# Kernel tuning notes

Measured on AMD Instinct MI355X. Metric: run time of the kernel, lower is better.

Reference implementation:

```python
import jax, jax.numpy as jnp
import numpy as np

HIDDEN = 300
DEPTH = 6
ATOM_FDIM = 136
BOND_FDIM = 12
BOND_IN = ATOM_FDIM + BOND_FDIM  # 148
MAX_NB = 6
N_MOLS = 4096
ATOMS_PER_MOL = 32
N_ATOMS = N_MOLS * ATOMS_PER_MOL  # 131072
N_BONDS = 2 * N_ATOMS            # 262144 directed bonds


def setup_inputs() -> dict:
    key = jax.random.key(0)
    ks = jax.random.split(key, 11)
    fatoms = jax.random.normal(ks[0], (N_ATOMS, ATOM_FDIM), jnp.float32)
    fbonds = jax.random.normal(ks[1], (N_BONDS, BOND_IN), jnp.float32)
    agraph = jax.random.randint(ks[2], (N_ATOMS, MAX_NB), 0, N_BONDS, jnp.int32)
    bgraph = jax.random.randint(ks[3], (N_BONDS, MAX_NB), 0, N_BONDS, jnp.int32)
    # Linear weights stored pre-transposed so forward is x @ W
    W_i = jax.random.normal(ks[4], (BOND_IN, HIDDEN), jnp.float32) / np.sqrt(BOND_IN)
    W_h = jax.random.normal(ks[5], (HIDDEN, HIDDEN), jnp.float32) / np.sqrt(HIDDEN)
    W_o = jax.random.normal(ks[6], (ATOM_FDIM + HIDDEN, HIDDEN), jnp.float32) / np.sqrt(ATOM_FDIM + HIDDEN)
    b_o = jax.random.normal(ks[7], (HIDDEN,), jnp.float32) * 0.01
    W_a = jax.random.normal(ks[8], (HIDDEN, HIDDEN), jnp.float32) / np.sqrt(HIDDEN)
    W_b = jax.random.normal(ks[9], (HIDDEN, HIDDEN), jnp.float32) / np.sqrt(HIDDEN)
    b_b = jax.random.normal(ks[10], (HIDDEN,), jnp.float32) * 0.01
    return {"fatoms": fatoms, "fbonds": fbonds, "agraph": agraph, "bgraph": bgraph,
            "W_i": W_i, "W_h": W_h, "W_o": W_o, "b_o": b_o,
            "W_a": W_a, "W_b": W_b, "b_b": b_b}


def reference(fatoms, fbonds, agraph, bgraph, W_i, W_h, W_o, b_o, W_a, W_b, b_b):
    # D-MPNN bond message passing (dropout=0.0 -> identity)
    binput = fbonds @ W_i                         # [N_b, H]
    message = jax.nn.relu(binput)
    for _ in range(DEPTH - 1):
        nei = jnp.take(message, bgraph, axis=0).sum(axis=1)   # gather [N_b, MAX_NB, H] -> sum
        message = jax.nn.relu(binput + nei @ W_h)
    nei_a = jnp.take(message, agraph, axis=0).sum(axis=1)     # [N_a, H]
    atom_hiddens = jax.nn.relu(jnp.concatenate([fatoms, nei_a], axis=1) @ W_o + b_o)
    # Per-molecule self-attention pooling (fixed-size scope: ATOMS_PER_MOL atoms/mol)
    h = atom_hiddens.reshape(N_MOLS, ATOMS_PER_MOL, HIDDEN)   # [B, A, H]
    q = jnp.einsum('bah,hk->bak', h, W_a)
    att = jax.nn.softmax(jnp.einsum('bak,bck->bac', q, h), axis=-1)
    att_h = jax.nn.relu(jnp.einsum('bac,bch->bah', att, h) @ W_b + b_b)
    mol_vecs = (h + att_h).sum(axis=1) / ATOMS_PER_MOL        # [B, H]
    return mol_vecs
```

## Files before the change

### kernel.cpp

```cpp
#include <hip/hip_runtime.h>
#include <hip/hip_fp16.h>
#include <math.h>

#define HIDDEN 300
#define ATOM_FDIM 136
#define BOND_IN 148
#define MAX_NB 6
#define N_MOLS 4096
#define APM 32
#define N_ATOMS (N_MOLS*APM)
#define N_BONDS (2*N_ATOMS)

#define BK 16
#define BM 64
#define ASTR 68
#define BSTR 304

#define WT_C 304
#define WTK_H 320
#define WTK_O 448

typedef unsigned short u16;
typedef short bf16x8 __attribute__((ext_vector_type(8)));
typedef float f32x4  __attribute__((ext_vector_type(4)));

__device__ float g_scratch[3ull * N_BONDS * HIDDEN / 2 + 3ull * N_ATOMS * HIDDEN
                           + (size_t)N_MOLS * HIDDEN + WT_C * (WTK_H + WTK_O)];

__device__ __forceinline__ u16 bf16_rne(float x) {
    unsigned u = __float_as_uint(x);
    unsigned r = (u + 0x7fffu + ((u >> 16) & 1u)) >> 16;
    return (u16)r;
}
__device__ __forceinline__ float bf16_f(u16 h) {
    return __uint_as_float(((unsigned)h) << 16);
}
__device__ __forceinline__ void st_h4(__half* p, float a, float b, float c, float d) {
    *(__half2*)(p)     = __floats2half2_rn(a, b);
    *(__half2*)(p + 2) = __floats2half2_rn(c, d);
}

__global__ __launch_bounds__(256)
void wt_prep(const float* __restrict__ W, u16* __restrict__ hi_out,
             u16* __restrict__ lo_out, int kact, int wtk)
{
    const int i = blockIdx.x * 256 + threadIdx.x;
    if (i >= WT_C * wtk) return;
    const int c = i / wtk, k = i - c * wtk;
    float w = (c < HIDDEN && k < kact) ? W[(size_t)k * HIDDEN + c] : 0.f;
    const u16 hi = bf16_rne(w);
    const u16 lo = bf16_rne(w - bf16_f(hi));
    hi_out[i] = hi;
    lo_out[i] = lo;
}

__global__ __launch_bounds__(512)
void mp_mfma(const __half* __restrict__ msg,
             const int*   __restrict__ graph,
             const u16*   __restrict__ wt_hi,
             const u16*   __restrict__ wt_lo,
             const __half* __restrict__ binput,
             __half* __restrict__ out0)
{
    __shared__ u16 Ahi[64 * 40];
    __shared__ u16 Alo[64 * 40];
    __shared__ int gx[64 * MAX_NB];

    const int tid  = threadIdx.x;
    const int row0 = blockIdx.x * 64;

    if (tid < 64 * MAX_NB) gx[tid] = graph[(size_t)row0 * MAX_NB + tid];
    __syncthreads();

    const int w  = tid >> 6;
    const int l  = tid & 63;
    const int g  = l >> 4;
    const int mr = (w & 3) * 16 + (l & 15);
    const int tbase = (w >> 2) ? 10 : 0;
    const int ntile = (w >> 2) ? 9 : 10;

    const int sr = tid >> 3;
    const int sk = (tid & 7) * 4;
    const int* sg = &gx[sr * MAX_NB];

    f32x4 acc[10];
#pragma unroll
    for (int t = 0; t < 10; ++t) acc[t] = (f32x4){0.f, 0.f, 0.f, 0.f};

    for (int k0 = 0; k0 < HIDDEN; k0 += 32) {
        const int kk = k0 + sk;
        float s0 = 0.f, s1 = 0.f, s2 = 0.f, s3 = 0.f;
#pragma unroll
        for (int j = 0; j < MAX_NB; ++j) {
            const __half2* p = (const __half2*)(msg + (size_t)sg[j] * HIDDEN + kk);
            const float2 u = __half22float2(p[0]);
            const float2 v = __half22float2(p[1]);
            s0 += u.x; s1 += u.y; s2 += v.x; s3 += v.y;
        }
        const u16 h0 = bf16_rne(s0), h1 = bf16_rne(s1), h2 = bf16_rne(s2), h3 = bf16_rne(s3);
        const u16 e0 = bf16_rne(s0 - bf16_f(h0)), e1 = bf16_rne(s1 - bf16_f(h1));
        const u16 e2 = bf16_rne(s2 - bf16_f(h2)), e3 = bf16_rne(s3 - bf16_f(h3));
        uint2 ph, pl;
        ph.x = (unsigned)h0 | ((unsigned)h1 << 16);
        ph.y = (unsigned)h2 | ((unsigned)h3 << 16);
        pl.x = (unsigned)e0 | ((unsigned)e1 << 16);
        pl.y = (unsigned)e2 | ((unsigned)e3 << 16);
        *(uint2*)&Ahi[sr * 40 + sk] = ph;
        *(uint2*)&Alo[sr * 40 + sk] = pl;
        __syncthreads();

        const bf16x8 ahi = *(const bf16x8*)&Ahi[mr * 40 + 8 * g];
        const bf16x8 alo = *(const bf16x8*)&Alo[mr * 40 + 8 * g];
        const int kb = k0 + 8 * g;

#pragma unroll
        for (int t = 0; t < 10; ++t) {
            if (t < ntile) {
                const int cn = 16 * (tbase + t) + (l & 15);
                const bf16x8 bhi = *(const bf16x8*)&wt_hi[(size_t)cn * WTK_H + kb];
                const bf16x8 blo = *(const bf16x8*)&wt_lo[(size_t)cn * WTK_H + kb];
                acc[t] = __builtin_amdgcn_mfma_f32_16x16x32_bf16(ahi, bhi, acc[t], 0, 0, 0);
                acc[t] = __builtin_amdgcn_mfma_f32_16x16x32_bf16(ahi, blo, acc[t], 0, 0, 0);
                acc[t] = __builtin_amdgcn_mfma_f32_16x16x32_bf16(alo, bhi, acc[t], 0, 0, 0);
            }
        }
        __syncthreads();
    }

#pragma unroll
    for (int t = 0; t < 10; ++t) {
        if (t < ntile) {
            const int col = 16 * (tbase + t) + (l & 15);
            if (col < HIDDEN) {
#pragma unroll
                for (int j = 0; j < 4; ++j) {
                    const size_t off = (size_t)(row0 + (w & 3) * 16 + 4 * g + j) * HIDDEN + col;
                    out0[off] = __float2half(fmaxf(__half2float(binput[off]) + acc[t][j], 0.f));
                }
            }
        }
    }
}

__global__ __launch_bounds__(512)
void mo_mfma(const float* __restrict__ fatoms,
             const __half* __restrict__ msg,
             const int*   __restrict__ graph,
             const u16*   __restrict__ wto_hi,
             const u16*   __restrict__ wto_lo,
             const float* __restrict__ bias,
             float* __restrict__ out0)
{
    __shared__ u16 Ahi[64 * 40];
    __shared__ u16 Alo[64 * 40];
    __shared__ int gx[64 * MAX_NB];

    const int tid  = threadIdx.x;
    const int row0 = blockIdx.x * 64;

    if (tid < 64 * MAX_NB) gx[tid] = graph[(size_t)row0 * MAX_NB + tid];
    __syncthreads();

    const int w  = tid >> 6;
    const int l  = tid & 63;
    const int g  = l >> 4;
    const int mr = (w & 3) * 16 + (l & 15);
    const int tbase = (w >> 2) ? 10 : 0;
    const int ntile = (w >> 2) ? 9 : 10;

    const int sr = tid >> 3;
    const int sk = (tid & 7) * 4;
    const int* sg = &gx[sr * MAX_NB];
    const float* fa = fatoms + (size_t)(row0 + sr) * ATOM_FDIM;

    f32x4 acc[10];
#pragma unroll
    for (int t = 0; t < 10; ++t) acc[t] = (f32x4){0.f, 0.f, 0.f, 0.f};

    for (int k0 = 0; k0 < WTK_O; k0 += 32) {
        const int kk = k0 + sk;
        float s0, s1, s2, s3;
        if (kk + 4 <= ATOM_FDIM) {
            const float4 v = *(const float4*)&fa[kk];
            s0 = v.x; s1 = v.y; s2 = v.z; s3 = v.w;
        } else {
            const int kg = kk - ATOM_FDIM;
            s0 = 0.f; s1 = 0.f; s2 = 0.f; s3 = 0.f;
#pragma unroll
            for (int j = 0; j < MAX_NB; ++j) {
                const __half2* p = (const __half2*)(msg + (size_t)sg[j] * HIDDEN + kg);
                const float2 u = __half22float2(p[0]);
                const float2 v = __half22float2(p[1]);
                s0 += u.x; s1 += u.y; s2 += v.x; s3 += v.y;
            }
        }
        const u16 h0 = bf16_rne(s0), h1 = bf16_rne(s1), h2 = bf16_rne(s2), h3 = bf16_rne(s3);
        const u16 e0 = bf16_rne(s0 - bf16_f(h0)), e1 = bf16_rne(s1 - bf16_f(h1));
        const u16 e2 = bf16_rne(s2 - bf16_f(h2)), e3 = bf16_rne(s3 - bf16_f(h3));
        uint2 ph, pl;
        ph.x = (unsigned)h0 | ((unsigned)h1 << 16);
        ph.y = (unsigned)h2 | ((unsigned)h3 << 16);
        pl.x = (unsigned)e0 | ((unsigned)e1 << 16);
        pl.y = (unsigned)e2 | ((unsigned)e3 << 16);
        *(uint2*)&Ahi[sr * 40 + sk] = ph;
        *(uint2*)&Alo[sr * 40 + sk] = pl;
        __syncthreads();

        const bf16x8 ahi = *(const bf16x8*)&Ahi[mr * 40 + 8 * g];
        const bf16x8 alo = *(const bf16x8*)&Alo[mr * 40 + 8 * g];
        const int kb = k0 + 8 * g;

#pragma unroll
        for (int t = 0; t < 10; ++t) {
            if (t < ntile) {
                const int cn = 16 * (tbase + t) + (l & 15);
                const bf16x8 bhi = *(const bf16x8*)&wto_hi[(size_t)cn * WTK_O + kb];
                const bf16x8 blo = *(const bf16x8*)&wto_lo[(size_t)cn * WTK_O + kb];
                acc[t] = __builtin_amdgcn_mfma_f32_16x16x32_bf16(ahi, bhi, acc[t], 0, 0, 0);
                acc[t] = __builtin_amdgcn_mfma_f32_16x16x32_bf16(ahi, blo, acc[t], 0, 0, 0);
                acc[t] = __builtin_amdgcn_mfma_f32_16x16x32_bf16(alo, bhi, acc[t], 0, 0, 0);
            }
        }
        __syncthreads();
    }

#pragma unroll
    for (int t = 0; t < 10; ++t) {
        if (t < ntile) {
            const int col = 16 * (tbase + t) + (l & 15);
            if (col < HIDDEN) {
                const float bv = bias[col];
#pragma unroll
                for (int j = 0; j < 4; ++j) {
                    const size_t off = (size_t)(row0 + (w & 3) * 16 + 4 * g + j) * HIDDEN + col;
                    out0[off] = fmaxf(acc[t][j] + bv, 0.f);
                }
            }
        }
    }
}

template<int MODE>
__global__ __launch_bounds__(512)
void gemm_fused(const float* __restrict__ Adense, int lda,
                const float* __restrict__ W,
                const float* __restrict__ bias,
                const float* __restrict__ hsum,
                float* __restrict__ out0,
                float* __restrict__ out1,
                int K)
{
    __shared__ float As[BK * ASTR];
    __shared__ float Bs[BK * BSTR];

    const int tid  = threadIdx.x;
    const int wave = tid >> 6;
    const int lane = tid & 63;
    const int row0 = blockIdx.x * BM;
    const int c0   = 4 * lane;
    const bool has4 = (lane < HIDDEN - 256);
    const int  c4   = has4 ? (256 + lane) : 256;

    float acc[8][5];
#pragma unroll
    for (int r = 0; r < 8; ++r)
#pragma unroll
        for (int c = 0; c < 5; ++c) acc[r][c] = 0.f;

    const int nk = (K + BK - 1) / BK;
    for (int kt = 0; kt < nk; ++kt) {
        const int k0 = kt * BK;
        for (int i = tid; i < BK * 300; i += 512) {
            const int kk = i / 300;
            const int col = i - kk * 300;
            const int k = k0 + kk;
            Bs[kk * BSTR + col] = (k < K) ? W[(size_t)k * HIDDEN + col] : 0.f;
        }
        for (int i = tid; i < BK * BM; i += 512) {
            const int r  = i >> 4;
            const int kk = i & 15;
            const int k  = k0 + kk;
            As[kk * ASTR + r] = (k < K) ? Adense[(size_t)(row0 + r) * lda + k] : 0.f;
        }
        __syncthreads();
#pragma unroll
        for (int kk = 0; kk < BK; ++kk) {
            const float4 bq = *(const float4*)&Bs[kk * BSTR + c0];
            const float  b4 = Bs[kk * BSTR + c4];
            const float4 a0 = *(const float4*)&As[kk * ASTR + wave * 8];
            const float4 a1 = *(const float4*)&As[kk * ASTR + wave * 8 + 4];
            const float ar8[8] = {a0.x, a0.y, a0.z, a0.w, a1.x, a1.y, a1.z, a1.w};
#pragma unroll
            for (int r = 0; r < 8; ++r) {
                acc[r][0] = fmaf(ar8[r], bq.x, acc[r][0]);
                acc[r][1] = fmaf(ar8[r], bq.y, acc[r][1]);
                acc[r][2] = fmaf(ar8[r], bq.z, acc[r][2]);
                acc[r][3] = fmaf(ar8[r], bq.w, acc[r][3]);
                acc[r][4] = fmaf(ar8[r], b4,   acc[r][4]);
            }
        }
        __syncthreads();
    }

    if (MODE == 4) {
        const float4 bqv = *(const float4*)&bias[c0];
        const float  b4v = bias[c4];
        float s0 = 0, s1 = 0, s2 = 0, s3 = 0, s4 = 0;
#pragma unroll
        for (int r = 0; r < 8; ++r) {
            s0 += fmaxf(acc[r][0] + bqv.x, 0.f);
            s1 += fmaxf(acc[r][1] + bqv.y, 0.f);
            s2 += fmaxf(acc[r][2] + bqv.z, 0.f);
            s3 += fmaxf(acc[r][3] + bqv.w, 0.f);
            s4 += fmaxf(acc[r][4] + b4v,   0.f);
        }
        float* wsum = Bs;
        *(float4*)&wsum[wave * BSTR + c0] = make_float4(s0, s1, s2, s3);
        if (has4) wsum[wave * BSTR + c4] = s4;
        __syncthreads();
        const int m0 = blockIdx.x * 2;
        for (int t = tid; t < 2 * HIDDEN; t += 512) {
            const int m = t / HIDDEN, col = t - m * HIDDEN;
            const float v = wsum[(4 * m + 0) * BSTR + col] + wsum[(4 * m + 1) * BSTR + col]
                          + wsum[(4 * m + 2) * BSTR + col] + wsum[(4 * m + 3) * BSTR + col]
                          + hsum[(size_t)(m0 + m) * HIDDEN + col];
            out0[(size_t)(m0 + m) * HIDDEN + col] = v * (1.f / 32.f);
        }
        return;
    }

#pragma unroll
    for (int r = 0; r < 8; ++r) {
        const size_t off = (size_t)(row0 + wave * 8 + r) * HIDDEN;
        float4 v = make_float4(acc[r][0], acc[r][1], acc[r][2], acc[r][3]);
        float v4 = acc[r][4];
        if (MODE == 0) {
            __half* o0 = (__half*)out0;
            __half* o1 = (__half*)out1;
            st_h4(&o0[off + c0], v.x, v.y, v.z, v.w);
            if (has4) o0[off + c4] = __float2half(v4);
            st_h4(&o1[off + c0], fmaxf(v.x,0.f), fmaxf(v.y,0.f), fmaxf(v.z,0.f), fmaxf(v.w,0.f));
            if (has4) o1[off + c4] = __float2half(fmaxf(v4, 0.f));
        } else {
            *(float4*)&out0[off + c0] = v;
            if (has4) out0[off + c4] = v4;
        }
    }
}

#define HSTR 320

__device__ __forceinline__ int hsw(int a, int c4u) {
    return a * HSTR + ((c4u ^ (a & 7)) << 2);
}

__global__ __launch_bounds__(512)
void attn_mid(const float* __restrict__ atom_h,
              const float* __restrict__ q_all,
              float* __restrict__ P_all,
              float* __restrict__ hsum)
{
    __shared__ float hs[APM * HSTR];
    __shared__ float qs[APM * HIDDEN];
    __shared__ float att[APM][33];

    const int tid  = threadIdx.x;
    const int wave = tid >> 6;
    const int lane = tid & 63;
    const int mol  = blockIdx.x;
    const float* hb = atom_h + (size_t)mol * APM * HIDDEN;
    const float* qb = q_all  + (size_t)mol * APM * HIDDEN;

    for (int j = tid; j < APM * 75; j += 512) {
        const int a = j / 75, c4u = j - a * 75;
        *(float4*)&hs[hsw(a, c4u)] = *(const float4*)&hb[(size_t)a * HIDDEN + 4 * c4u];
    }
    for (int j = tid; j < APM * 75; j += 512)
        *(float4*)&qs[4 * j] = *(const float4*)&qb[4 * j];
    __syncthreads();

    {
        const int a = tid >> 5, b = tid & 31;
        float s0 = 0.f, s1 = 0.f;
        for (int t = 0; t < 75; ++t) {
            const float4 hv = *(const float4*)&hs[hsw(b, t)];
            const float4 q0 = *(const float4*)&qs[a * HIDDEN + 4 * t];
            const float4 q1 = *(const float4*)&qs[(a + 16) * HIDDEN + 4 * t];
            s0 = fmaf(q0.x, hv.x, fmaf(q0.y, hv.y, fmaf(q0.z, hv.z, fmaf(q0.w, hv.w, s0))));
            s1 = fmaf(q1.x, hv.x, fmaf(q1.y, hv.y, fmaf(q1.z, hv.z, fmaf(q1.w, hv.w, s1))));
        }
        att[a][b] = s0;
        att[a + 16][b] = s1;
    }
    __syncthreads();

    if (tid < APM) {
        float m = -3.4e38f;
#pragma unroll 4
        for (int b = 0; b < APM; ++b) m = fmaxf(m, att[tid][b]);
        float s = 0.f;
#pragma unroll 4
        for (int b = 0; b < APM; ++b) { const float e = __expf(att[tid][b] - m); att[tid][b] = e; s += e; }
        const float inv = 1.f / s;
#pragma unroll 4
        for (int b = 0; b < APM; ++b) att[tid][b] *= inv;
    }
    __syncthreads();

    {
        const int r0 = wave * 4;
        const int c0 = 4 * lane;
        const bool has4 = (lane < 44);
        const int c4u = 64 + (lane >> 2), c4r = lane & 3;
        float4 p[4];
        float  p4[4];
#pragma unroll
        for (int r = 0; r < 4; ++r) { p[r] = make_float4(0,0,0,0); p4[r] = 0.f; }
#pragma unroll 4
        for (int b = 0; b < APM; ++b) {
            const float4 hv = *(const float4*)&hs[hsw(b, lane)];
            const float  h4 = hs[hsw(b, c4u) + c4r];
#pragma unroll
            for (int r = 0; r < 4; ++r) {
                const float av = att[r0 + r][b];
                p[r].x = fmaf(av, hv.x, p[r].x);
                p[r].y = fmaf(av, hv.y, p[r].y);
                p[r].z = fmaf(av, hv.z, p[r].z);
                p[r].w = fmaf(av, hv.w, p[r].w);
                p4[r]  = fmaf(av, h4,   p4[r]);
            }
        }
#pragma unroll
        for (int r = 0; r < 4; ++r) {
            const size_t off = ((size_t)mol * APM + r0 + r) * HIDDEN;
            *(float4*)&P_all[off + c0] = p[r];
            if (has4) P_all[off + 256 + lane] = p4[r];
        }
    }

    if (tid < HIDDEN) {
        const int c4u = tid >> 2, cr = tid & 3;
        float s = 0.f;
#pragma unroll 4
        for (int a = 0; a < APM; ++a) s += hs[hsw(a, c4u) + cr];
        hsum[(size_t)mol * HIDDEN + tid] = s;
    }
}

extern "C" void kernel_launch(void* const* d_in, const int* in_sizes, int n_in,
                              void* d_out, int out_size, void* d_ws, size_t ws_size,
                              hipStream_t stream)
{
    const float* fatoms = (const float*)d_in[0];
    const float* fbonds = (const float*)d_in[1];
    const int*   agraph = (const int*)d_in[2];
    const int*   bgraph = (const int*)d_in[3];
    const float* W_i    = (const float*)d_in[4];
    const float* W_h    = (const float*)d_in[5];
    const float* W_o    = (const float*)d_in[6];
    const float* b_o    = (const float*)d_in[7];
    const float* W_a    = (const float*)d_in[8];
    const float* W_b    = (const float*)d_in[9];
    const float* b_b    = (const float*)d_in[10];
    float* out = (float*)d_out;

    const size_t WB = (size_t)N_BONDS * HIDDEN;
    const size_t WA = (size_t)N_ATOMS * HIDDEN;
    const size_t need = (3 * WB / 2 + 3 * WA + (size_t)N_MOLS * HIDDEN
                         + WT_C * (WTK_H + WTK_O)) * sizeof(float);
    float* base;
    if (ws_size >= need) {
        base = (float*)d_ws;
    } else {
        void* p = nullptr;
        (void)hipGetSymbolAddress(&p, HIP_SYMBOL(g_scratch));
        base = (float*)p;
    }
    __half* binput_h = (__half*)base;
    __half* msgA     = (__half*)(base + WB / 2);
    __half* msgB     = (__half*)(base + WB);
    float*  atom_h   = base + 3 * WB / 2;
    float*  q_all    = atom_h + WA;
    float*  P_all    = q_all + WA;
    float*  hsum     = P_all + WA;
    u16*    wt_hi    = (u16*)(hsum + (size_t)N_MOLS * HIDDEN);
    u16*    wt_lo    = wt_hi + WT_C * WTK_H;
    u16*    wto_hi   = wt_lo + WT_C * WTK_H;
    u16*    wto_lo   = wto_hi + WT_C * WTK_O;

    const dim3 blk(512);

    wt_prep<<<(WT_C * WTK_H + 255) / 256, dim3(256), 0, stream>>>(
        W_h, wt_hi, wt_lo, HIDDEN, WTK_H);
    wt_prep<<<(WT_C * WTK_O + 255) / 256, dim3(256), 0, stream>>>(
        W_o, wto_hi, wto_lo, ATOM_FDIM + HIDDEN, WTK_O);

    gemm_fused<0><<<N_BONDS / BM, blk, 0, stream>>>(
        fbonds, BOND_IN, W_i, nullptr, nullptr,
        (float*)binput_h, (float*)msgA, BOND_IN);

    const __half* cur = msgA;
    __half* nxt = msgB;
    for (int it = 0; it < 5; ++it) {
        mp_mfma<<<N_BONDS / 64, blk, 0, stream>>>(
            cur, bgraph, wt_hi, wt_lo, binput_h, nxt);
        __half* t = nxt; nxt = (__half*)cur; cur = t;
    }

    mo_mfma<<<N_ATOMS / 64, blk, 0, stream>>>(
        fatoms, cur, agraph, wto_hi, wto_lo, b_o, atom_h);

    gemm_fused<3><<<N_ATOMS / BM, blk, 0, stream>>>(
        atom_h, HIDDEN, W_a, nullptr, nullptr,
        q_all, nullptr, HIDDEN);

    attn_mid<<<N_MOLS, dim3(512), 0, stream>>>(atom_h, q_all, P_all, hsum);

    gemm_fused<4><<<N_ATOMS / BM, blk, 0, stream>>>(
        P_all, HIDDEN, W_b, b_b, hsum,
        out, nullptr, HIDDEN);
}
```

Baseline: 6.711 ms.

## Replace FP32 SIMT GEMMs with split-bf16 MFMA kernels for W_i, W_a, W_b

```diff
diff --git a/kernel.cpp b/kernel.cpp
--- a/kernel.cpp
+++ b/kernel.cpp
@@ -11,21 +11,17 @@
 #define N_ATOMS (N_MOLS*APM)
 #define N_BONDS (2*N_ATOMS)
 
-#define BK 16
-#define BM 64
-#define ASTR 68
-#define BSTR 304
-
 #define WT_C 304
 #define WTK_H 320
 #define WTK_O 448
+#define WTK_I 160
 
 typedef unsigned short u16;
 typedef short bf16x8 __attribute__((ext_vector_type(8)));
 typedef float f32x4  __attribute__((ext_vector_type(4)));
 
 __device__ float g_scratch[3ull * N_BONDS * HIDDEN / 2 + 3ull * N_ATOMS * HIDDEN
-                           + (size_t)N_MOLS * HIDDEN + WT_C * (WTK_H + WTK_O)];
+                           + (size_t)N_MOLS * HIDDEN + 476672];
 
 __device__ __forceinline__ u16 bf16_rne(float x) {
     unsigned u = __float_as_uint(x);
@@ -34,10 +30,6 @@
 }
 __device__ __forceinline__ float bf16_f(u16 h) {
     return __uint_as_float(((unsigned)h) << 16);
-}
-__device__ __forceinline__ void st_h4(__half* p, float a, float b, float c, float d) {
-    *(__half2*)(p)     = __floats2half2_rn(a, b);
-    *(__half2*)(p + 2) = __floats2half2_rn(c, d);
 }
 
 __global__ __launch_bounds__(256)
@@ -54,6 +46,18 @@
     lo_out[i] = lo;
 }
 
+__device__ __forceinline__ void split4(float s0, float s1, float s2, float s3,
+                                       uint2& ph, uint2& pl)
+{
+    const u16 h0 = bf16_rne(s0), h1 = bf16_rne(s1), h2 = bf16_rne(s2), h3 = bf16_rne(s3);
+    const u16 e0 = bf16_rne(s0 - bf16_f(h0)), e1 = bf16_rne(s1 - bf16_f(h1));
+    const u16 e2 = bf16_rne(s2 - bf16_f(h2)), e3 = bf16_rne(s3 - bf16_f(h3));
+    ph.x = (unsigned)h0 | ((unsigned)h1 << 16);
+    ph.y = (unsigned)h2 | ((unsigned)h3 << 16);
+    pl.x = (unsigned)e0 | ((unsigned)e1 << 16);
+    pl.y = (unsigned)e2 | ((unsigned)e3 << 16);
+}
+
 __global__ __launch_bounds__(512)
 void mp_mfma(const __half* __restrict__ msg,
              const int*   __restrict__ graph,
@@ -97,14 +101,8 @@
             const float2 v = __half22float2(p[1]);
             s0 += u.x; s1 += u.y; s2 += v.x; s3 += v.y;
         }
-        const u16 h0 = bf16_rne(s0), h1 = bf16_rne(s1), h2 = bf16_rne(s2), h3 = bf16_rne(s3);
-        const u16 e0 = bf16_rne(s0 - bf16_f(h0)), e1 = bf16_rne(s1 - bf16_f(h1));
-        const u16 e2 = bf16_rne(s2 - bf16_f(h2)), e3 = bf16_rne(s3 - bf16_f(h3));
         uint2 ph, pl;
-        ph.x = (unsigned)h0 | ((unsigned)h1 << 16);
-        ph.y = (unsigned)h2 | ((unsigned)h3 << 16);
-        pl.x = (unsigned)e0 | ((unsigned)e1 << 16);
-        pl.y = (unsigned)e2 | ((unsigned)e3 << 16);
+        split4(s0, s1, s2, s3, ph, pl);
         *(uint2*)&Ahi[sr * 40 + sk] = ph;
         *(uint2*)&Alo[sr * 40 + sk] = pl;
         __syncthreads();
@@ -194,14 +192,8 @@
                 s0 += u.x; s1 += u.y; s2 += v.x; s3 += v.y;
             }
         }
-        const u16 h0 = bf16_rne(s0), h1 = bf16_rne(s1), h2 = bf16_rne(s2), h3 = bf16_rne(s3);
-        const u16 e0 = bf16_rne(s0 - bf16_f(h0)), e1 = bf16_rne(s1 - bf16_f(h1));
-        const u16 e2 = bf16_rne(s2 - bf16_f(h2)), e3 = bf16_rne(s3 - bf16_f(h3));
         uint2 ph, pl;
-        ph.x = (unsigned)h0 | ((unsigned)h1 << 16);
-        ph.y = (unsigned)h2 | ((unsigned)h3 << 16);
-        pl.x = (unsigned)e0 | ((unsigned)e1 << 16);
-        pl.y = (unsigned)e2 | ((unsigned)e3 << 16);
+        split4(s0, s1, s2, s3, ph, pl);
         *(uint2*)&Ahi[sr * 40 + sk] = ph;
         *(uint2*)&Alo[sr * 40 + sk] = pl;
         __syncthreads();
@@ -242,108 +234,114 @@
 
 template<int MODE>
 __global__ __launch_bounds__(512)
-void gemm_fused(const float* __restrict__ Adense, int lda,
-                const float* __restrict__ W,
-                const float* __restrict__ bias,
-                const float* __restrict__ hsum,
-                float* __restrict__ out0,
-                float* __restrict__ out1,
-                int K)
-{
-    __shared__ float As[BK * ASTR];
-    __shared__ float Bs[BK * BSTR];
+void gd_mfma(const float* __restrict__ A,
+             const u16* __restrict__ wt_hi,
+             const u16* __restrict__ wt_lo,
+             const float* __restrict__ bias,
+             const float* __restrict__ hsum,
+             float* __restrict__ out0,
+             float* __restrict__ out1)
+{
+    constexpr int K    = (MODE == 0) ? BOND_IN : HIDDEN;
+    constexpr int KPAD = (MODE == 0) ? WTK_I : WTK_H;
+
+    __shared__ u16 Ahi[64 * 40];
+    __shared__ u16 Alo[64 * 40];
 
     const int tid  = threadIdx.x;
-    const int wave = tid >> 6;
-    const int lane = tid & 63;
-    const int row0 = blockIdx.x * BM;
-    const int c0   = 4 * lane;
-    const bool has4 = (lane < HIDDEN - 256);
-    const int  c4   = has4 ? (256 + lane) : 256;
-
-    float acc[8][5];
-#pragma unroll
-    for (int r = 0; r < 8; ++r)
-#pragma unroll
-        for (int c = 0; c < 5; ++c) acc[r][c] = 0.f;
-
-    const int nk = (K + BK - 1) / BK;
-    for (int kt = 0; kt < nk; ++kt) {
-        const int k0 = kt * BK;
-        for (int i = tid; i < BK * 300; i += 512) {
-            const int kk = i / 300;
-            const int col = i - kk * 300;
-            const int k = k0 + kk;
-            Bs[kk * BSTR + col] = (k < K) ? W[(size_t)k * HIDDEN + col] : 0.f;
-        }
-        for (int i = tid; i < BK * BM; i += 512) {
-            const int r  = i >> 4;
-            const int kk = i & 15;
-            const int k  = k0 + kk;
-            As[kk * ASTR + r] = (k < K) ? Adense[(size_t)(row0 + r) * lda + k] : 0.f;
-        }
-        __syncthreads();
-#pragma unroll
-        for (int kk = 0; kk < BK; ++kk) {
-            const float4 bq = *(const float4*)&Bs[kk * BSTR + c0];
-            const float  b4 = Bs[kk * BSTR + c4];
-            const float4 a0 = *(const float4*)&As[kk * ASTR + wave * 8];
-            const float4 a1 = *(const float4*)&As[kk * ASTR + wave * 8 + 4];
-            const float ar8[8] = {a0.x, a0.y, a0.z, a0.w, a1.x, a1.y, a1.z, a1.w};
-#pragma unroll
-            for (int r = 0; r < 8; ++r) {
-                acc[r][0] = fmaf(ar8[r], bq.x, acc[r][0]);
-                acc[r][1] = fmaf(ar8[r], bq.y, acc[r][1]);
-                acc[r][2] = fmaf(ar8[r], bq.z, acc[r][2]);
-                acc[r][3] = fmaf(ar8[r], bq.w, acc[r][3]);
-                acc[r][4] = fmaf(ar8[r], b4,   acc[r][4]);
-            }
-        }
-        __syncthreads();
-    }
-
-    if (MODE == 4) {
-        const float4 bqv = *(const float4*)&bias[c0];
-        const float  b4v = bias[c4];
-        float s0 = 0, s1 = 0, s2 = 0, s3 = 0, s4 = 0;
-#pragma unroll
-        for (int r = 0; r < 8; ++r) {
-            s0 += fmaxf(acc[r][0] + bqv.x, 0.f);
-            s1 += fmaxf(acc[r][1] + bqv.y, 0.f);
-            s2 += fmaxf(acc[r][2] + bqv.z, 0.f);
-            s3 += fmaxf(acc[r][3] + bqv.w, 0.f);
-            s4 += fmaxf(acc[r][4] + b4v,   0.f);
-        }
-        float* wsum = Bs;
-        *(float4*)&wsum[wave * BSTR + c0] = make_float4(s0, s1, s2, s3);
-        if (has4) wsum[wave * BSTR + c4] = s4;
+    const int row0 = blockIdx.x * 64;
+
+    const int w  = tid >> 6;
+    const int l  = tid & 63;
+    const int g  = l >> 4;
+    const int mr = (w & 3) * 16 + (l & 15);
+    const int tbase = (w >> 2) ? 10 : 0;
+    const int ntile = (w >> 2) ? 9 : 10;
+
+    const int sr = tid >> 3;
+    const int sk = (tid & 7) * 4;
+    const float* ar = A + (size_t)(row0 + sr) * K;
+
+    f32x4 acc[10];
+#pragma unroll
+    for (int t = 0; t < 10; ++t) acc[t] = (f32x4){0.f, 0.f, 0.f, 0.f};
+
+    for (int k0 = 0; k0 < KPAD; k0 += 32) {
+        const int kk = k0 + sk;
+        float s0 = 0.f, s1 = 0.f, s2 = 0.f, s3 = 0.f;
+        if (kk + 4 <= K) {
+            const float4 v = *(const float4*)&ar[kk];
+            s0 = v.x; s1 = v.y; s2 = v.z; s3 = v.w;
+        }
+        uint2 ph, pl;
+        split4(s0, s1, s2, s3, ph, pl);
+        *(uint2*)&Ahi[sr * 40 + sk] = ph;
+        *(uint2*)&Alo[sr * 40 + sk] = pl;
+        __syncthreads();
+
+        const bf16x8 ahi = *(const bf16x8*)&Ahi[mr * 40 + 8 * g];
+        const bf16x8 alo = *(const bf16x8*)&Alo[mr * 40 + 8 * g];
+        const int kb = k0 + 8 * g;
+
+#pragma unroll
+        for (int t = 0; t < 10; ++t) {
+            if (t < ntile) {
+                const int cn = 16 * (tbase + t) + (l & 15);
+                const bf16x8 bhi = *(const bf16x8*)&wt_hi[(size_t)cn * KPAD + kb];
+                const bf16x8 blo = *(const bf16x8*)&wt_lo[(size_t)cn * KPAD + kb];
+                acc[t] = __builtin_amdgcn_mfma_f32_16x16x32_bf16(ahi, bhi, acc[t], 0, 0, 0);
+                acc[t] = __builtin_amdgcn_mfma_f32_16x16x32_bf16(ahi, blo, acc[t], 0, 0, 0);
+                acc[t] = __builtin_amdgcn_mfma_f32_16x16x32_bf16(alo, bhi, acc[t], 0, 0, 0);
+            }
+        }
+        __syncthreads();
+    }
+
+    if constexpr (MODE == 4) {
+        __shared__ float part[2][8][304];
+        const int m    = (w & 3) >> 1;
+        const int cidx = ((w & 3) & 1) * 4 + g;
+#pragma unroll
+        for (int t = 0; t < 10; ++t) {
+            if (t < ntile) {
+                const int col = 16 * (tbase + t) + (l & 15);
+                const float bv = bias[col < HIDDEN ? col : 0];
+                float s = 0.f;
+#pragma unroll
+                for (int j = 0; j < 4; ++j) s += fmaxf(acc[t][j] + bv, 0.f);
+                part[m][cidx][col] = s;
+            }
+        }
         __syncthreads();
         const int m0 = blockIdx.x * 2;
-        for (int t = tid; t < 2 * HIDDEN; t += 512) {
-            const int m = t / HIDDEN, col = t - m * HIDDEN;
-            const float v = wsum[(4 * m + 0) * BSTR + col] + wsum[(4 * m + 1) * BSTR + col]
-                          + wsum[(4 * m + 2) * BSTR + col] + wsum[(4 * m + 3) * BSTR + col]
-                          + hsum[(size_t)(m0 + m) * HIDDEN + col];
-            out0[(size_t)(m0 + m) * HIDDEN + col] = v * (1.f / 32.f);
+        for (int t2 = tid; t2 < 2 * HIDDEN; t2 += 512) {
+            const int mm = t2 / HIDDEN, col = t2 - mm * HIDDEN;
+            float s = 0.f;
+#pragma unroll
+            for (int c = 0; c < 8; ++c) s += part[mm][c][col];
+            const size_t o = (size_t)(m0 + mm) * HIDDEN + col;
+            out0[o] = (s + hsum[o]) * (1.f / 32.f);
         }
         return;
     }
 
 #pragma unroll
-    for (int r = 0; r < 8; ++r) {
-        const size_t off = (size_t)(row0 + wave * 8 + r) * HIDDEN;
-        float4 v = make_float4(acc[r][0], acc[r][1], acc[r][2], acc[r][3]);
-        float v4 = acc[r][4];
-        if (MODE == 0) {
-            __half* o0 = (__half*)out0;
-            __half* o1 = (__half*)out1;
-            st_h4(&o0[off + c0], v.x, v.y, v.z, v.w);
-            if (has4) o0[off + c4] = __float2half(v4);
-            st_h4(&o1[off + c0], fmaxf(v.x,0.f), fmaxf(v.y,0.f), fmaxf(v.z,0.f), fmaxf(v.w,0.f));
-            if (has4) o1[off + c4] = __float2half(fmaxf(v4, 0.f));
-        } else {
-            *(float4*)&out0[off + c0] = v;
-            if (has4) out0[off + c4] = v4;
+    for (int t = 0; t < 10; ++t) {
+        if (t < ntile) {
+            const int col = 16 * (tbase + t) + (l & 15);
+            if (col < HIDDEN) {
+#pragma unroll
+                for (int j = 0; j < 4; ++j) {
+                    const size_t off = (size_t)(row0 + (w & 3) * 16 + 4 * g + j) * HIDDEN + col;
+                    const float v = acc[t][j];
+                    if (MODE == 0) {
+                        ((__half*)out0)[off] = __float2half(v);
+                        ((__half*)out1)[off] = __float2half(fmaxf(v, 0.f));
+                    } else {
+                        out0[off] = v;
+                    }
+                }
+            }
         }
     }
 }
@@ -466,8 +464,7 @@
 
     const size_t WB = (size_t)N_BONDS * HIDDEN;
     const size_t WA = (size_t)N_ATOMS * HIDDEN;
-    const size_t need = (3 * WB / 2 + 3 * WA + (size_t)N_MOLS * HIDDEN
-                         + WT_C * (WTK_H + WTK_O)) * sizeof(float);
+    const size_t need = (3 * WB / 2 + 3 * WA + (size_t)N_MOLS * HIDDEN + 476672) * sizeof(float);
     float* base;
     if (ws_size >= need) {
         base = (float*)d_ws;
@@ -483,40 +480,45 @@
     float*  q_all    = atom_h + WA;
     float*  P_all    = q_all + WA;
     float*  hsum     = P_all + WA;
-    u16*    wt_hi    = (u16*)(hsum + (size_t)N_MOLS * HIDDEN);
-    u16*    wt_lo    = wt_hi + WT_C * WTK_H;
-    u16*    wto_hi   = wt_lo + WT_C * WTK_H;
+    u16*    wth_hi   = (u16*)(hsum + (size_t)N_MOLS * HIDDEN);
+    u16*    wth_lo   = wth_hi + WT_C * WTK_H;
+    u16*    wto_hi   = wth_lo + WT_C * WTK_H;
     u16*    wto_lo   = wto_hi + WT_C * WTK_O;
+    u16*    wti_hi   = wto_lo + WT_C * WTK_O;
+    u16*    wti_lo   = wti_hi + WT_C * WTK_I;
+    u16*    wta_hi   = wti_lo + WT_C * WTK_I;
+    u16*    wta_lo   = wta_hi + WT_C * WTK_H;
+    u16*    wtb_hi   = wta_lo + WT_C * WTK_H;
+    u16*    wtb_lo   = wtb_hi + WT_C * WTK_H;
 
     const dim3 blk(512);
 
-    wt_prep<<<(WT_C * WTK_H + 255) / 256, dim3(256), 0, stream>>>(
-        W_h, wt_hi, wt_lo, HIDDEN, WTK_H);
-    wt_prep<<<(WT_C * WTK_O + 255) / 256, dim3(256), 0, stream>>>(
-        W_o, wto_hi, wto_lo, ATOM_FDIM + HIDDEN, WTK_O);
-
-    gemm_fused<0><<<N_BONDS / BM, blk, 0, stream>>>(
-        fbonds, BOND_IN, W_i, nullptr, nullptr,
-        (float*)binput_h, (float*)msgA, BOND_IN);
+    wt_prep<<<(WT_C * WTK_H + 255) / 256, dim3(256), 0, stream>>>(W_h, wth_hi, wth_lo, HIDDEN, WTK_H);
+    wt_prep<<<(WT_C * WTK_O + 255) / 256, dim3(256), 0, stream>>>(W_o, wto_hi, wto_lo, ATOM_FDIM + HIDDEN, WTK_O);
+    wt_prep<<<(WT_C * WTK_I + 255) / 256, dim3(256), 0, stream>>>(W_i, wti_hi, wti_lo, BOND_IN, WTK_I);
+    wt_prep<<<(WT_C * WTK_H + 255) / 256, dim3(256), 0, stream>>>(W_a, wta_hi, wta_lo, HIDDEN, WTK_H);
+    wt_prep<<<(WT_C * WTK_H + 255) / 256, dim3(256), 0, stream>>>(W_b, wtb_hi, wtb_lo, HIDDEN, WTK_H);
+
+    gd_mfma<0><<<N_BONDS / 64, blk, 0, stream>>>(
+        fbonds, wti_hi, wti_lo, nullptr, nullptr,
+        (float*)binput_h, (float*)msgA);
 
     const __half* cur = msgA;
     __half* nxt = msgB;
     for (int it = 0; it < 5; ++it) {
         mp_mfma<<<N_BONDS / 64, blk, 0, stream>>>(
-            cur, bgraph, wt_hi, wt_lo, binput_h, nxt);
+            cur, bgraph, wth_hi, wth_lo, binput_h, nxt);
         __half* t = nxt; nxt = (__half*)cur; cur = t;
     }
 
     mo_mfma<<<N_ATOMS / 64, blk, 0, stream>>>(
         fatoms, cur, agraph, wto_hi, wto_lo, b_o, atom_h);
 
-    gemm_fused<3><<<N_ATOMS / BM, blk, 0, stream>>>(
-        atom_h, HIDDEN, W_a, nullptr, nullptr,
-        q_all, nullptr, HIDDEN);
+    gd_mfma<3><<<N_ATOMS / 64, blk, 0, stream>>>(
+        atom_h, wta_hi, wta_lo, nullptr, nullptr, q_all, nullptr);
 
     attn_mid<<<N_MOLS, dim3(512), 0, stream>>>(atom_h, q_all, P_all, hsum);
 
-    gemm_fused<4><<<N_ATOMS / BM, blk, 0, stream>>>(
-        P_all, HIDDEN, W_b, b_b, hsum,
-        out, nullptr, HIDDEN);
-}
+    gd_mfma<4><<<N_ATOMS / 64, blk, 0, stream>>>(
+        P_all, wtb_hi, wtb_lo, b_b, hsum, out, nullptr);
+}
```

After: 6.260 ms. 1.07x faster.
